# Optimization experiments

Hardware: AMD Instinct MI355X
Metric: run time of the kernel (lower is better)

## Reference

```python
import jax, jax.numpy as jnp
import numpy as np

MARGIN = 0.1
NEG_FLOOR = 0.6  # max(0.6, hardest_pos) threshold from the original code


def setup_inputs() -> dict:
    key = jax.random.key(0)
    k1, k2 = jax.random.split(key)
    n, d, n_classes = 8192, 128, 512
    emb = jax.random.normal(k1, (n, d), dtype=jnp.float32)
    target = jax.random.randint(k2, (n,), 0, n_classes, dtype=jnp.int64)
    return {"emb": emb, "target": target}


def reference(emb, target):
    n = emb.shape[0]
    # L2-normalize embeddings (F.normalize with eps=1e-12 clamp on the norm)
    norm = jnp.linalg.norm(emb, axis=-1, keepdims=True)
    e = emb / jnp.maximum(norm, 1e-12)
    sim = e @ e.T  # [n, n] cosine similarity

    same = target[:, None] == target[None, :]
    eye = jnp.eye(n, dtype=bool)
    pos_mask = same & ~eye
    neg_mask = ~same

    neg_inf = jnp.float32(-jnp.inf)
    # hardest (largest-sim) negative and positive per row; sorting in the
    # original only serves to grab these maxima and apply thresholds.
    max_neg = jnp.max(jnp.where(neg_mask, sim, neg_inf), axis=1)  # [n]
    max_pos = jnp.max(jnp.where(pos_mask, sim, neg_inf), axis=1)  # [n]

    has_pos = jnp.any(pos_mask, axis=1)  # rows with no positive contribute 0

    # positives with sim < hardest_neg + margin (hard positives)
    pos_sel = pos_mask & (sim < (max_neg + MARGIN)[:, None])
    pos_loss = jnp.sum(jnp.where(pos_sel, 1.0 - sim, 0.0), axis=1)

    # negatives with sim > max(0.6, hardest_pos) - margin (hard negatives)
    thr = jnp.maximum(jnp.float32(NEG_FLOOR), max_pos) - MARGIN
    neg_sel = neg_mask & (sim > thr[:, None])
    neg_loss = jnp.sum(jnp.where(neg_sel, sim, 0.0), axis=1)

    row_loss = jnp.where(has_pos, pos_loss + neg_loss, 0.0)
    return jnp.sum(row_loss) / n
```

## Files before the change

### kernel.cpp

```cpp
#include <hip/hip_runtime.h>


#define D 128
#define NCLS 512
#define CAP 2048
#define PSIM_CAP (512 * 1024)
#define MARGIN 0.1f
#define NEG_FLOOR 0.6f
#define NINF -1e30f

typedef short bf16x8 __attribute__((ext_vector_type(8)));
typedef float f32x4 __attribute__((ext_vector_type(4)));

__device__ __forceinline__ unsigned short f2bf(float f) {
  unsigned u = __float_as_uint(f);
  u += 0x7FFFu + ((u >> 16) & 1u);
  return (unsigned short)(u >> 16);
}

__device__ __forceinline__ unsigned fenc(float f) {
  unsigned u = __float_as_uint(f);
  return (u & 0x80000000u) ? ~u : (u | 0x80000000u);
}
__device__ __forceinline__ float fdec(unsigned e) {
  unsigned u = (e & 0x80000000u) ? (e & 0x7FFFFFFFu) : ~e;
  return __uint_as_float(u);
}

__device__ __forceinline__ void push_cand(unsigned* cnt,
                                          unsigned long long* cand, int row,
                                          float s) {
  unsigned idx = atomicAdd(cnt, 1u);
  if (idx < CAP)
    cand[idx] = ((unsigned long long)(unsigned)row << 32) | __float_as_uint(s);
}

__global__ void k_histrank(const int* __restrict__ tgt, int* __restrict__ H,
                           int* __restrict__ rnk,
                           unsigned* __restrict__ maxNegEnc,
                           unsigned* __restrict__ cnt) {
  __shared__ int cls[128];
  __shared__ int h[NCLS];
  const int chunk = blockIdx.x;
  const int tid = threadIdx.x;
  const int i = chunk * 128 + tid;
  if (chunk == 0 && tid == 0) *cnt = 0u;
  cls[tid] = tgt[i];
  for (int k = tid; k < NCLS; k += 128) h[k] = 0;
  __syncthreads();
  const int c = cls[tid];
  atomicAdd(&h[c], 1);
  int r = 0;
  for (int j = 0; j < tid; ++j) r += (cls[j] == c);
  rnk[i] = r;
  maxNegEnc[i] = 0u;
  __syncthreads();
  for (int k = tid; k < NCLS; k += 128) H[chunk * NCLS + k] = h[k];
}

__global__ void k_scan(const int* __restrict__ H, int* __restrict__ CB,
                       int* __restrict__ cls_start, int* __restrict__ pbase,
                       int n) {
  __shared__ int wsum[8], wsum2[8];
  const int c = threadIdx.x;
  int t = 0;
#pragma unroll 8
  for (int k = 0; k < 64; ++k) t += H[k * NCLS + c];
  const int t2 = t * t;
  const int lane = c & 63, w = c >> 6;
  int v = t, v2 = t2;
#pragma unroll
  for (int off = 1; off < 64; off <<= 1) {
    int u = __shfl_up(v, off, 64);
    int u2 = __shfl_up(v2, off, 64);
    if (lane >= off) {
      v += u;
      v2 += u2;
    }
  }
  if (lane == 63) {
    wsum[w] = v;
    wsum2[w] = v2;
  }
  __syncthreads();
  if (c < 8) {
    int x = wsum[c], x2 = wsum2[c];
#pragma unroll
    for (int off = 1; off < 8; off <<= 1) {
      int u = __shfl_up(x, off, 64);
      int u2 = __shfl_up(x2, off, 64);
      if (lane >= off) {
        x += u;
        x2 += u2;
      }
    }
    wsum[c] = x;
    wsum2[c] = x2;
  }
  __syncthreads();
  int base = v + ((w > 0) ? wsum[w - 1] : 0) - t;
  int base2 = v2 + ((w > 0) ? wsum2[w - 1] : 0) - t2;
  cls_start[c] = base;
  if (c == NCLS - 1) cls_start[NCLS] = n;
  pbase[c] = base2;
  int run = base;
#pragma unroll 8
  for (int k = 0; k < 64; ++k) {
    CB[k * NCLS + c] = run;
    run += H[k * NCLS + c];
  }
}

__global__ void k_normS(const float* __restrict__ emb,
                        const int* __restrict__ tgt,
                        const int* __restrict__ rnk, const int* __restrict__ CB,
                        const int* __restrict__ cls_start,
                        const int* __restrict__ pbase, uint4* __restrict__ ebB,
                        int* __restrict__ tgtS, int* __restrict__ rowS0,
                        int* __restrict__ rowM, int* __restrict__ rowBase,
                        int n) {
  const int s = blockIdx.x;
  const int rl = threadIdx.x >> 4;
  const int c16 = threadIdx.x & 15;
  const int orig = s * 16 + rl;
  const float* q = emb + (size_t)orig * D + c16 * 8;
  float4 v0 = *(const float4*)q;
  float4 v1 = *(const float4*)(q + 4);
  float ss = v0.x * v0.x + v0.y * v0.y + v0.z * v0.z + v0.w * v0.w +
             v1.x * v1.x + v1.y * v1.y + v1.z * v1.z + v1.w * v1.w;
#pragma unroll
  for (int off = 1; off < 16; off <<= 1) ss += __shfl_xor(ss, off, 64);
  float invn = 1.0f / fmaxf(sqrtf(ss), 1e-12f);
  uint4 wv;
  wv.x = (unsigned)f2bf(v0.x * invn) | ((unsigned)f2bf(v0.y * invn) << 16);
  wv.y = (unsigned)f2bf(v0.z * invn) | ((unsigned)f2bf(v0.w * invn) << 16);
  wv.z = (unsigned)f2bf(v1.x * invn) | ((unsigned)f2bf(v1.y * invn) << 16);
  wv.w = (unsigned)f2bf(v1.z * invn) | ((unsigned)f2bf(v1.w * invn) << 16);
  const int cls = tgt[orig];
  const int chunk = orig >> 7;
  const int pos = CB[chunk * NCLS + cls] + rnk[orig];
  const int sstripe = pos >> 4, srl = pos & 15;
  const int ks = c16 >> 2, g = c16 & 3;
  ebB[((sstripe * 4 + ks) * 64) + (g * 16 + srl)] = wv;
  if (c16 == 0) {
    int s0 = cls_start[cls];
    tgtS[pos] = cls;
    rowS0[pos] = s0;
    rowM[pos] = cls_start[cls + 1] - s0;
    rowBase[pos] = pbase[cls];
  }
}

__global__ __launch_bounds__(512, 2) void k_passN(
    const bf16x8* __restrict__ ebB, const int* __restrict__ tgtS,
    const int* __restrict__ rowS0, const int* __restrict__ rowM,
    const int* __restrict__ rowBase, float* __restrict__ psim,
    unsigned* __restrict__ maxNegEnc, unsigned* __restrict__ cnt,
    unsigned long long* __restrict__ cand, int n) {
  __shared__ char Bs[32768];
  __shared__ float colbuf[8][8][16];
  __shared__ int sBuf[16];

  const int tid = threadIdx.x;
  const int lane = tid & 63;
  const int w = tid >> 6;
  const int l15 = lane & 15, g = lane >> 4;

  const int nby = n >> 7;
  int t = blockIdx.x, bi = 0, rem = nby;
  while (t >= rem) {
    t -= rem;
    ++bi;
    rem -= 2;
  }
  const int bj = 2 * bi + t;
  const bool colside = (bj >= 2 * bi + 2);
  const int cs0 = bj * 8;
  const int rbase = bi * 256 + w * 32;

  {
    const char* src = (const char*)ebB + (size_t)cs0 * 4096;
#pragma unroll
    for (int i = 0; i < 4; ++i) {
      __builtin_amdgcn_global_load_lds(
          (const __attribute__((address_space(1))) void*)(src + i * 8192 +
                                                          tid * 16),
          (__attribute__((address_space(3))) void*)(Bs + i * 8192 + tid * 16),
          16, 0, 0);
    }
  }
  if (tid < 16) {
    int si = tid >> 1, which = tid & 1;
    sBuf[tid] = tgtS[(cs0 + si) * 16 + which * 15];
  }

  const int sA = rbase >> 4;
  const int clo = tgtS[rbase], chi = tgtS[rbase + 31];

  bf16x8 a[2][4];
#pragma unroll
  for (int mt = 0; mt < 2; ++mt)
#pragma unroll
    for (int ks = 0; ks < 4; ++ks)
      a[mt][ks] = ebB[((sA + mt) * 4 + ks) * 64 + lane];

  float accN[2][4];
#pragma unroll
  for (int mt = 0; mt < 2; ++mt)
#pragma unroll
    for (int r = 0; r < 4; ++r) accN[mt][r] = NINF;

  __syncthreads();

#pragma unroll 1
  for (int si = 0; si < 8; ++si) {
    const int cs = cs0 + si;
    bf16x8 b[4];
#pragma unroll
    for (int ks = 0; ks < 4; ++ks)
      b[ks] = *(const bf16x8*)(Bs + si * 4096 + ks * 1024 + lane * 16);
    const int slo = sBuf[2 * si], shi = sBuf[2 * si + 1];

    f32x4 acc[2];
#pragma unroll
    for (int mt = 0; mt < 2; ++mt) acc[mt] = (f32x4){0.f, 0.f, 0.f, 0.f};
    __builtin_amdgcn_s_setprio(1);
#pragma unroll
    for (int ks = 0; ks < 4; ++ks)
#pragma unroll
      for (int mt = 0; mt < 2; ++mt)
        acc[mt] = __builtin_amdgcn_mfma_f32_16x16x32_bf16(a[mt][ks], b[ks],
                                                          acc[mt], 0, 0, 0);
    __builtin_amdgcn_s_setprio(0);

    const bool dirty = (clo <= shi) && (slo <= chi);
    float colMax;
    if (!dirty) {
#pragma unroll
      for (int mt = 0; mt < 2; ++mt)
#pragma unroll
        for (int r = 0; r < 4; ++r)
          accN[mt][r] = fmaxf(accN[mt][r], acc[mt][r]);
      float m0x =
          fmaxf(fmaxf(acc[0][0], acc[0][1]), fmaxf(acc[0][2], acc[0][3]));
      float m1x =
          fmaxf(fmaxf(acc[1][0], acc[1][1]), fmaxf(acc[1][2], acc[1][3]));
      colMax = fmaxf(m0x, m1x);
      if (__any(colMax > 0.5f)) {
#pragma unroll
        for (int mt = 0; mt < 2; ++mt)
#pragma unroll
          for (int r = 0; r < 4; ++r)
            if (acc[mt][r] > 0.5f) {
              int row = rbase + mt * 16 + g * 4 + r;
              int col = cs * 16 + l15;
              push_cand(cnt, cand, row, acc[mt][r]);
              if (colside) push_cand(cnt, cand, col, acc[mt][r]);
            }
      }
    } else {
      const int tc = tgtS[cs * 16 + l15];
      const int col = cs * 16 + l15;
      int4 ta = *(const int4*)(tgtS + rbase + g * 4);
      int4 tb = *(const int4*)(tgtS + rbase + 16 + g * 4);
      int tr[2][4] = {{ta.x, ta.y, ta.z, ta.w}, {tb.x, tb.y, tb.z, tb.w}};
      colMax = NINF;
#pragma unroll
      for (int mt = 0; mt < 2; ++mt)
#pragma unroll
        for (int r = 0; r < 4; ++r) {
          float s = acc[mt][r];
          const int row = rbase + mt * 16 + g * 4 + r;
          if (tr[mt][r] == tc) {
            int s0 = rowS0[row];
            int m = rowM[row];
            int b0 = rowBase[row];
            psim[b0 + (row - s0) * m + (col - s0)] = s;
            if (colside) psim[b0 + (col - s0) * m + (row - s0)] = s;
          } else {
            accN[mt][r] = fmaxf(accN[mt][r], s);
            colMax = fmaxf(colMax, s);
            if (s > 0.5f) {
              push_cand(cnt, cand, row, s);
              if (colside) push_cand(cnt, cand, col, s);
            }
          }
        }
    }
    if (colside) {
      float v = fmaxf(colMax, __shfl_xor(colMax, 16, 64));
      v = fmaxf(v, __shfl_xor(v, 32, 64));
      if (lane < 16) colbuf[si][w][l15] = v;
    }
  }

#pragma unroll
  for (int mt = 0; mt < 2; ++mt)
#pragma unroll
    for (int r = 0; r < 4; ++r) {
      float vn = accN[mt][r];
#pragma unroll
      for (int off = 1; off < 16; off <<= 1)
        vn = fmaxf(vn, __shfl_xor(vn, off, 64));
      if (l15 == 0)
        atomicMax(&maxNegEnc[rbase + mt * 16 + g * 4 + r], fenc(vn));
    }

  if (colside) {
    __syncthreads();
    if (tid < 128) {
      int si = tid >> 4, l = tid & 15;
      float v = colbuf[si][0][l];
#pragma unroll
      for (int k = 1; k < 8; ++k) v = fmaxf(v, colbuf[si][k][l]);
      atomicMax(&maxNegEnc[(cs0 + si) * 16 + l], fenc(v));
    }
  }
}

__global__ void k_stats(const float* __restrict__ psim,
                        const int* __restrict__ rowS0,
                        const int* __restrict__ rowM,
                        const int* __restrict__ rowBase,
                        const unsigned* __restrict__ maxNegEnc,
                        float* __restrict__ thrNeg, float* __restrict__ bpart,
                        int n) {
  __shared__ float red[256];
  int p = blockIdx.x * 256 + threadIdx.x;
  float contrib = 0.f;
  int m = rowM[p];
  if (m <= 1) {
    thrNeg[p] = 1e30f;
  } else {
    float tp = fdec(maxNegEnc[p]) + MARGIN;
    int i = p - rowS0[p];
    const float* row = psim + rowBase[p] + (size_t)i * m;
    float mp = NINF, pl = 0.f;
    for (int j = 0; j < m; ++j) {
      if (j == i) continue;
      float s = row[j];
      mp = fmaxf(mp, s);
      pl += (s < tp) ? (1.f - s) : 0.f;
    }
    thrNeg[p] = fmaxf(NEG_FLOOR, mp) - MARGIN;
    contrib = pl;
  }
  red[threadIdx.x] = contrib;
  __syncthreads();
  for (int off = 128; off > 0; off >>= 1) {
    if ((int)threadIdx.x < off) red[threadIdx.x] += red[threadIdx.x + off];
    __syncthreads();
  }
  if (threadIdx.x == 0) bpart[blockIdx.x] = red[0];
}

__global__ void k_fix(const unsigned* __restrict__ cnt,
                      const unsigned long long* __restrict__ cand,
                      const float* __restrict__ thrNeg,
                      const float* __restrict__ bpart, float* __restrict__ out,
                      int n, int nb) {
  __shared__ unsigned long long buf[CAP];
  __shared__ unsigned long long srt[CAP];
  int k = (int)min(*cnt, (unsigned)CAP);
  for (int i = threadIdx.x; i < k; i += 256) buf[i] = cand[i];
  __syncthreads();
  for (int i = threadIdx.x; i < k; i += 256) {
    unsigned long long v = buf[i];
    int rk = 0;
    for (int j = 0; j < k; ++j) {
      unsigned long long u = buf[j];
      rk += (u < v) || (u == v && j < i);
    }
    srt[rk] = v;
  }
  __syncthreads();
  if (threadIdx.x == 0) {
    float tot = 0.f;
    for (int i = 0; i < nb; ++i) tot += bpart[i];
    for (int i = 0; i < k; ++i) {
      int row = (int)(srt[i] >> 32);
      float s = __uint_as_float((unsigned)srt[i]);
      if (s > thrNeg[row]) tot += s;
    }
    out[0] = tot / (float)n;
  }
}

extern "C" void kernel_launch(void* const* d_in, const int* in_sizes, int n_in,
                              void* d_out, int out_size, void* d_ws,
                              size_t ws_size, hipStream_t stream) {
  const float* emb = (const float*)d_in[0];
  const int* tgt = (const int*)d_in[1];
  float* out = (float*)d_out;
  const int n = in_sizes[1];

  char* ws = (char*)d_ws;
  uint4* ebB = (uint4*)ws;
  float* psim = (float*)(ws + (size_t)n * D * 2);
  unsigned long long* cand = (unsigned long long*)(psim + PSIM_CAP);
  float* thrNeg = (float*)(cand + CAP);
  float* bpart = thrNeg + n;
  unsigned* maxNegEnc = (unsigned*)(bpart + 64);
  unsigned* cnt = maxNegEnc + n;
  int* cls_start = (int*)(cnt + 64);
  int* pbase = cls_start + 1024;
  int* H = pbase + 1024;
  int* CB = H + 64 * NCLS;
  int* rnk = CB + 64 * NCLS;
  int* tgtS = rnk + n;
  int* rowS0 = tgtS + n;
  int* rowM = rowS0 + n;
  int* rowBase = rowM + n;

  k_histrank<<<n / 128, 128, 0, stream>>>(tgt, H, rnk, maxNegEnc, cnt);
  k_scan<<<1, NCLS, 0, stream>>>(H, CB, cls_start, pbase, n);
  k_normS<<<n / 16, 256, 0, stream>>>(emb, tgt, rnk, CB, cls_start, pbase,
                                      ebB, tgtS, rowS0, rowM, rowBase, n);

  const int nbx = n / 256, nby = n / 128;
  const int tblocks = nbx * nby - nbx * (nbx - 1);
  k_passN<<<tblocks, 512, 0, stream>>>((const bf16x8*)ebB, tgtS, rowS0, rowM,
                                       rowBase, psim, maxNegEnc, cnt, cand,
                                       n);
  k_stats<<<n / 256, 256, 0, stream>>>(psim, rowS0, rowM, rowBase, maxNegEnc,
                                       thrNeg, bpart, n);
  k_fix<<<1, 256, 0, stream>>>(cnt, cand, thrNeg, bpart, out, n, n / 256);
}
```

Baseline: 60.36 us.

## Replace candidate atomics with recompute of hard-negative rows in fix kernel

```diff
diff --git a/kernel.cpp b/kernel.cpp
--- a/kernel.cpp
+++ b/kernel.cpp
@@ -3,7 +3,7 @@
 
 #define D 128
 #define NCLS 512
-#define CAP 2048
+#define FCAP 256
 #define PSIM_CAP (512 * 1024)
 #define MARGIN 0.1f
 #define NEG_FLOOR 0.6f
@@ -27,24 +27,14 @@
   return __uint_as_float(u);
 }
 
-__device__ __forceinline__ void push_cand(unsigned* cnt,
-                                          unsigned long long* cand, int row,
-                                          float s) {
-  unsigned idx = atomicAdd(cnt, 1u);
-  if (idx < CAP)
-    cand[idx] = ((unsigned long long)(unsigned)row << 32) | __float_as_uint(s);
-}
-
 __global__ void k_histrank(const int* __restrict__ tgt, int* __restrict__ H,
                            int* __restrict__ rnk,
-                           unsigned* __restrict__ maxNegEnc,
-                           unsigned* __restrict__ cnt) {
+                           unsigned* __restrict__ maxNegEnc) {
   __shared__ int cls[128];
   __shared__ int h[NCLS];
   const int chunk = blockIdx.x;
   const int tid = threadIdx.x;
   const int i = chunk * 128 + tid;
-  if (chunk == 0 && tid == 0) *cnt = 0u;
   cls[tid] = tgt[i];
   for (int k = tid; k < NCLS; k += 128) h[k] = 0;
   __syncthreads();
@@ -155,8 +145,7 @@
     const bf16x8* __restrict__ ebB, const int* __restrict__ tgtS,
     const int* __restrict__ rowS0, const int* __restrict__ rowM,
     const int* __restrict__ rowBase, float* __restrict__ psim,
-    unsigned* __restrict__ maxNegEnc, unsigned* __restrict__ cnt,
-    unsigned long long* __restrict__ cand, int n) {
+    unsigned* __restrict__ maxNegEnc, int n) {
   __shared__ char Bs[32768];
   __shared__ float colbuf[8][8][16];
   __shared__ int sBuf[16];
@@ -234,29 +223,19 @@
     __builtin_amdgcn_s_setprio(0);
 
     const bool dirty = (clo <= shi) && (slo <= chi);
-    float colMax;
+    float colMax = NINF;
     if (!dirty) {
 #pragma unroll
       for (int mt = 0; mt < 2; ++mt)
 #pragma unroll
         for (int r = 0; r < 4; ++r)
           accN[mt][r] = fmaxf(accN[mt][r], acc[mt][r]);
-      float m0x =
-          fmaxf(fmaxf(acc[0][0], acc[0][1]), fmaxf(acc[0][2], acc[0][3]));
-      float m1x =
-          fmaxf(fmaxf(acc[1][0], acc[1][1]), fmaxf(acc[1][2], acc[1][3]));
-      colMax = fmaxf(m0x, m1x);
-      if (__any(colMax > 0.5f)) {
-#pragma unroll
-        for (int mt = 0; mt < 2; ++mt)
-#pragma unroll
-          for (int r = 0; r < 4; ++r)
-            if (acc[mt][r] > 0.5f) {
-              int row = rbase + mt * 16 + g * 4 + r;
-              int col = cs * 16 + l15;
-              push_cand(cnt, cand, row, acc[mt][r]);
-              if (colside) push_cand(cnt, cand, col, acc[mt][r]);
-            }
+      if (colside) {
+        float m0x =
+            fmaxf(fmaxf(acc[0][0], acc[0][1]), fmaxf(acc[0][2], acc[0][3]));
+        float m1x =
+            fmaxf(fmaxf(acc[1][0], acc[1][1]), fmaxf(acc[1][2], acc[1][3]));
+        colMax = fmaxf(m0x, m1x);
       }
     } else {
       const int tc = tgtS[cs * 16 + l15];
@@ -264,7 +243,6 @@
       int4 ta = *(const int4*)(tgtS + rbase + g * 4);
       int4 tb = *(const int4*)(tgtS + rbase + 16 + g * 4);
       int tr[2][4] = {{ta.x, ta.y, ta.z, ta.w}, {tb.x, tb.y, tb.z, tb.w}};
-      colMax = NINF;
 #pragma unroll
       for (int mt = 0; mt < 2; ++mt)
 #pragma unroll
@@ -280,10 +258,6 @@
           } else {
             accN[mt][r] = fmaxf(accN[mt][r], s);
             colMax = fmaxf(colMax, s);
-            if (s > 0.5f) {
-              push_cand(cnt, cand, row, s);
-              if (colside) push_cand(cnt, cand, col, s);
-            }
           }
         }
     }
@@ -354,36 +328,87 @@
   if (threadIdx.x == 0) bpart[blockIdx.x] = red[0];
 }
 
-__global__ void k_fix(const unsigned* __restrict__ cnt,
-                      const unsigned long long* __restrict__ cand,
+__global__ void k_fix(const uint4* __restrict__ ebB,
+                      const int* __restrict__ tgtS,
+                      const int* __restrict__ rowM,
+                      const unsigned* __restrict__ maxNegEnc,
                       const float* __restrict__ thrNeg,
                       const float* __restrict__ bpart, float* __restrict__ out,
                       int n, int nb) {
-  __shared__ unsigned long long buf[CAP];
-  __shared__ unsigned long long srt[CAP];
-  int k = (int)min(*cnt, (unsigned)CAP);
-  for (int i = threadIdx.x; i < k; i += 256) buf[i] = cand[i];
-  __syncthreads();
-  for (int i = threadIdx.x; i < k; i += 256) {
-    unsigned long long v = buf[i];
-    int rk = 0;
-    for (int j = 0; j < k; ++j) {
-      unsigned long long u = buf[j];
-      rk += (u < v) || (u == v && j < i);
-    }
-    srt[rk] = v;
-  }
-  __syncthreads();
-  if (threadIdx.x == 0) {
+  __shared__ int list[FCAP];
+  __shared__ unsigned lcnt;
+  __shared__ float rowbuf[128];
+  __shared__ float red[256];
+  __shared__ float totS;
+  const int tid = threadIdx.x;
+  if (tid == 0) lcnt = 0u;
+  __syncthreads();
+  for (int k = 0; k < 32; ++k) {
+    int p = tid * 32 + k;
+    if (rowM[p] > 1 && fdec(maxNegEnc[p]) > thrNeg[p]) {
+      unsigned idx = atomicAdd(&lcnt, 1u);
+      if (idx < FCAP) list[idx] = p;
+    }
+  }
+  __syncthreads();
+  int k = (int)min(lcnt, (unsigned)FCAP);
+  if (tid == 0) {
+    for (int i = 0; i < k; ++i)
+      for (int j = i + 1; j < k; ++j)
+        if (list[j] < list[i]) {
+          int tmp = list[i];
+          list[i] = list[j];
+          list[j] = tmp;
+        }
     float tot = 0.f;
     for (int i = 0; i < nb; ++i) tot += bpart[i];
-    for (int i = 0; i < k; ++i) {
-      int row = (int)(srt[i] >> 32);
-      float s = __uint_as_float((unsigned)srt[i]);
-      if (s > thrNeg[row]) tot += s;
-    }
-    out[0] = tot / (float)n;
-  }
+    totS = tot;
+  }
+  __syncthreads();
+  for (int ii = 0; ii < k; ++ii) {
+    const int p = list[ii];
+    if (tid < 16) {
+      int stripe = p >> 4, rl = p & 15, ks = tid >> 2, g = tid & 3;
+      uint4 v = ebB[(stripe * 4 + ks) * 64 + (g * 16 + rl)];
+      unsigned uu[4] = {v.x, v.y, v.z, v.w};
+#pragma unroll
+      for (int e = 0; e < 4; ++e) {
+        rowbuf[tid * 8 + e * 2] = __uint_as_float(uu[e] << 16);
+        rowbuf[tid * 8 + e * 2 + 1] = __uint_as_float(uu[e] & 0xFFFF0000u);
+      }
+    }
+    __syncthreads();
+    const int myCls = tgtS[p];
+    const float thr = thrNeg[p];
+    float acc = 0.f;
+    for (int c = tid * 32; c < tid * 32 + 32; ++c) {
+      if (tgtS[c] == myCls) continue;
+      int stripe = c >> 4, rl = c & 15;
+      float s = 0.f;
+#pragma unroll
+      for (int c16 = 0; c16 < 16; ++c16) {
+        int ks = c16 >> 2, g = c16 & 3;
+        uint4 v = ebB[(stripe * 4 + ks) * 64 + (g * 16 + rl)];
+        unsigned uu[4] = {v.x, v.y, v.z, v.w};
+#pragma unroll
+        for (int e = 0; e < 4; ++e) {
+          float b0 = __uint_as_float(uu[e] << 16);
+          float b1 = __uint_as_float(uu[e] & 0xFFFF0000u);
+          s += rowbuf[c16 * 8 + e * 2] * b0 + rowbuf[c16 * 8 + e * 2 + 1] * b1;
+        }
+      }
+      acc += (s > thr) ? s : 0.f;
+    }
+    red[tid] = acc;
+    __syncthreads();
+    for (int off = 128; off > 0; off >>= 1) {
+      if (tid < off) red[tid] += red[tid + off];
+      __syncthreads();
+    }
+    if (tid == 0) totS += red[0];
+    __syncthreads();
+  }
+  if (tid == 0) out[0] = totS / (float)n;
 }
 
 extern "C" void kernel_launch(void* const* d_in, const int* in_sizes, int n_in,
@@ -397,12 +422,10 @@
   char* ws = (char*)d_ws;
   uint4* ebB = (uint4*)ws;
   float* psim = (float*)(ws + (size_t)n * D * 2);
-  unsigned long long* cand = (unsigned long long*)(psim + PSIM_CAP);
-  float* thrNeg = (float*)(cand + CAP);
+  float* thrNeg = psim + PSIM_CAP;
   float* bpart = thrNeg + n;
   unsigned* maxNegEnc = (unsigned*)(bpart + 64);
-  unsigned* cnt = maxNegEnc + n;
-  int* cls_start = (int*)(cnt + 64);
+  int* cls_start = (int*)(maxNegEnc + n);
   int* pbase = cls_start + 1024;
   int* H = pbase + 1024;
   int* CB = H + 64 * NCLS;
@@ -412,7 +435,7 @@
   int* rowM = rowS0 + n;
   int* rowBase = rowM + n;
 
-  k_histrank<<<n / 128, 128, 0, stream>>>(tgt, H, rnk, maxNegEnc, cnt);
+  k_histrank<<<n / 128, 128, 0, stream>>>(tgt, H, rnk, maxNegEnc);
   k_scan<<<1, NCLS, 0, stream>>>(H, CB, cls_start, pbase, n);
   k_normS<<<n / 16, 256, 0, stream>>>(emb, tgt, rnk, CB, cls_start, pbase,
                                       ebB, tgtS, rowS0, rowM, rowBase, n);
@@ -420,9 +443,9 @@
   const int nbx = n / 256, nby = n / 128;
   const int tblocks = nbx * nby - nbx * (nbx - 1);
   k_passN<<<tblocks, 512, 0, stream>>>((const bf16x8*)ebB, tgtS, rowS0, rowM,
-                                       rowBase, psim, maxNegEnc, cnt, cand,
-                                       n);
+                                       rowBase, psim, maxNegEnc, n);
   k_stats<<<n / 256, 256, 0, stream>>>(psim, rowS0, rowM, rowBase, maxNegEnc,
                                        thrNeg, bpart, n);
-  k_fix<<<1, 256, 0, stream>>>(cnt, cand, thrNeg, bpart, out, n, n / 256);
-}
+  k_fix<<<1, 256, 0, stream>>>(ebB, tgtS, rowM, maxNegEnc, thrNeg, bpart, out,
+                               n, n / 256);
+}
```

Result: slower. 71.46 us (+18.4%).
